# Optimization experiments

Measured on AMD Instinct MI355X. Metric: run time of the kernel, lower is better.

The kernel has to match this reference:

```python
import jax, jax.numpy as jnp
import numpy as np

NC, EC, NS, ES = 100000, 1600000, 50000, 800000
F_IN, H, G, OUT = 7, 64, 1024, 2
EPS = 1e-5


def setup_inputs() -> dict:
    key = jax.random.key(0)
    ks = jax.random.split(key, 24)
    d = {
        'x_c': jax.random.normal(ks[0], (NC, F_IN), jnp.float32),
        'edge_index_c': jax.random.randint(ks[1], (2, EC), 0, NC),
        'batch_c': jnp.sort(jax.random.randint(ks[2], (NC,), 0, G)),
        'x_s': jax.random.normal(ks[3], (NS, F_IN), jnp.float32),
        'edge_index_s': jax.random.randint(ks[4], (2, ES), 0, NS),
        'batch_s': jnp.sort(jax.random.randint(ks[5], (NS,), 0, G)),
    }
    def lin(k, i, o):
        return jax.random.normal(k, (i, o), jnp.float32) * (1.0 / np.sqrt(i))
    # chromo branch layers
    d['Wc0'] = lin(ks[6], F_IN, H); d['bc0'] = jnp.zeros((H,), jnp.float32)
    d['gc0'] = jnp.ones((H,), jnp.float32); d['betac0'] = jnp.zeros((H,), jnp.float32)
    d['Wc1'] = lin(ks[7], H, H); d['bc1'] = jnp.zeros((H,), jnp.float32)
    d['gc1'] = jnp.ones((H,), jnp.float32); d['betac1'] = jnp.zeros((H,), jnp.float32)
    # solvent branch layers
    d['Ws0'] = lin(ks[8], F_IN, H); d['bs0'] = jnp.zeros((H,), jnp.float32)
    d['gs0'] = jnp.ones((H,), jnp.float32); d['betas0'] = jnp.zeros((H,), jnp.float32)
    d['Ws1'] = lin(ks[9], H, H); d['bs1'] = jnp.zeros((H,), jnp.float32)
    d['gs1'] = jnp.ones((H,), jnp.float32); d['betas1'] = jnp.zeros((H,), jnp.float32)
    # heads
    d['Wf1'] = lin(ks[10], 2 * H, H); d['bf1'] = jnp.zeros((H,), jnp.float32)
    d['Wf2'] = lin(ks[11], H, OUT); d['bf2'] = jnp.zeros((OUT,), jnp.float32)
    return d


def _gcn(x, src, dst, W, b):
    # PyG GCNConv: add self-loops, symmetric D^-1/2 (A+I) D^-1/2 normalization
    N = x.shape[0]
    xw = x @ W
    si = jnp.concatenate([src, jnp.arange(N)])
    di = jnp.concatenate([dst, jnp.arange(N)])
    deg = jax.ops.segment_sum(jnp.ones(si.shape[0], x.dtype), di, num_segments=N)
    dinv = jnp.where(deg > 0, jax.lax.rsqrt(jnp.maximum(deg, 1.0)), 0.0)
    msg = xw[si] * (dinv[si] * dinv[di])[:, None]
    return jax.ops.segment_sum(msg, di, num_segments=N) + b


def _bn_relu(x, g, b):
    mu = x.mean(0)
    var = x.var(0)
    return jax.nn.relu((x - mu) * jax.lax.rsqrt(var + EPS) * g + b)


def _branch(x, ei, batch, layers):
    for (W, b, g, bt) in layers:
        x = _bn_relu(_gcn(x, ei[0], ei[1], W, b), g, bt)
    s = jax.ops.segment_sum(x, batch, num_segments=G)
    cnt = jax.ops.segment_sum(jnp.ones(x.shape[0], x.dtype), batch, num_segments=G)
    return s / jnp.maximum(cnt, 1.0)[:, None]  # global_mean_pool


def reference(x_c, edge_index_c, batch_c, x_s, edge_index_s, batch_s,
              Wc0, bc0, gc0, betac0, Wc1, bc1, gc1, betac1,
              Ws0, bs0, gs0, betas0, Ws1, bs1, gs1, betas1,
              Wf1, bf1, Wf2, bf2):
    hc = _branch(x_c, edge_index_c, batch_c,
                 [(Wc0, bc0, gc0, betac0), (Wc1, bc1, gc1, betac1)])
    hs = _branch(x_s, edge_index_s, batch_s,
                 [(Ws0, bs0, gs0, betas0), (Ws1, bs1, gs1, betas1)])
    h = jnp.concatenate([hc, hs], axis=1)  # [G, 2H]
    h = jax.nn.relu(h @ Wf1 + bf1)
    return h @ Wf2 + bf2  # [G, 2]
```

## Files before the change

### kernel.cpp

```cpp
#include <hip/hip_runtime.h>
#include <hip/hip_bf16.h>

typedef __hip_bfloat16 bf16;
typedef __attribute__((ext_vector_type(8))) short short8;
typedef __attribute__((ext_vector_type(4))) float f32x4;

#define NC_ 100000
#define EC_ 1600000
#define NS_ 50000
#define ES_ 800000
#define G_  1024
#define EPS_ 1e-5f

#define NB_C 782
#define NB_S 391
#define NBMAX 782
#define KSL 16
#define CSR_WC 2000400
#define CSR_WS 1000208

#define WS_MIN_FALLBACK 39356176ull
#define WS_BIG          52163344ull

__device__ __forceinline__ float b2f(bf16 v) { return __bfloat162float(v); }

__device__ __forceinline__ unsigned short f2bfbits(float v) {
    bf16 b = __float2bfloat16(v);
    union { bf16 b; unsigned short u; } c; c.b = b; return c.u;
}

__device__ __forceinline__ void acc8(float* a, uint4 r) {
    a[0] += __uint_as_float(r.x << 16); a[1] += __uint_as_float(r.x & 0xffff0000u);
    a[2] += __uint_as_float(r.y << 16); a[3] += __uint_as_float(r.y & 0xffff0000u);
    a[4] += __uint_as_float(r.z << 16); a[5] += __uint_as_float(r.z & 0xffff0000u);
    a[6] += __uint_as_float(r.w << 16); a[7] += __uint_as_float(r.w & 0xffff0000u);
}

__global__ void DualGNN_31327491457689_kernel() {}

__global__ __launch_bounds__(256) void k_fillout(float* out, float val, int n) {
    int i = blockIdx.x * 256 + threadIdx.x;
    if (i < n) out[i] = val;
}

__global__ __launch_bounds__(256) void k_zero(int* p, int n) {
    int i = blockIdx.x * 256 + threadIdx.x;
    int stride = gridDim.x * 256;
    while (i < n) { p[i] = 0; i += stride; }
}

__global__ __launch_bounds__(256) void k_bhist2(const int* dst_c, int* bcnt_c,
                                                const int* dst_s, int* bcnt_s) {
    __shared__ int h[NBMAX];
    int t = threadIdx.x;
    const int* dst; int* bcnt; int E, NB, b0, nb;
    if (blockIdx.x < 256) { dst = dst_c; bcnt = bcnt_c; E = EC_; NB = NB_C; b0 = blockIdx.x; nb = 256; }
    else { dst = dst_s; bcnt = bcnt_s; E = ES_; NB = NB_S; b0 = blockIdx.x - 256; nb = 128; }
    for (int i = t; i < NB; i += 256) h[i] = 0;
    __syncthreads();
    for (int e = b0 * 256 + t; e < E; e += nb * 256)
        atomicAdd(&h[dst[e] >> 7], 1);
    __syncthreads();
    for (int i = t; i < NB; i += 256) {
        int v = h[i];
        if (v) atomicAdd(&bcnt[i], v);
    }
}

__device__ void scan_one(const int* cnt, int* base, int* cur, int NB, int (*sc)[1024]) {
    int t = threadIdx.x;
    for (int i = t; i < 1024; i += 256) sc[0][i] = (i < NB) ? cnt[i] : 0;
    __syncthreads();
    int pin = 0;
    for (int off = 1; off < 1024; off <<= 1) {
        for (int i = t; i < 1024; i += 256) {
            int v = sc[pin][i];
            if (i >= off) v += sc[pin][i - off];
            sc[1 - pin][i] = v;
        }
        __syncthreads();
        pin ^= 1;
    }
    for (int i = t; i <= NB; i += 256) {
        int e = (i == 0) ? 0 : sc[pin][i - 1];
        base[i] = e;
        if (i < NB) cur[i] = e;
    }
    __syncthreads();
}

__global__ __launch_bounds__(256) void k_bscan(const int* cnt_c, int* base_c, int* cur_c, int NBc,
                                               const int* cnt_s, int* base_s, int* cur_s, int NBs) {
    __shared__ int sc[2][1024];
    scan_one(cnt_c, base_c, cur_c, NBc, sc);
    scan_one(cnt_s, base_s, cur_s, NBs, sc);
}

__global__ __launch_bounds__(256) void k_bin2(const int* ei_c, int* bcur_c, int* ebuf_c,
                                              const int* ei_s, int* bcur_s, int* ebuf_s) {
    __shared__ int cnt[NBMAX];
    __shared__ int slot[NBMAX * KSL];
    int t = threadIdx.x;
    const int *src, *dst; int *bcur, *ebuf; int E, NB; int base;
    if (blockIdx.x < 391) {
        src = ei_c; dst = ei_c + EC_; bcur = bcur_c; ebuf = ebuf_c;
        E = EC_; NB = NB_C; base = blockIdx.x * 4096;
    } else {
        src = ei_s; dst = ei_s + ES_; bcur = bcur_s; ebuf = ebuf_s;
        E = ES_; NB = NB_S; base = (blockIdx.x - 391) * 4096;
    }
    if (base >= E) return;
    for (int i = t; i < NB; i += 256) cnt[i] = 0;
    __syncthreads();
    int e1 = base + 4096;
    if (e1 > E) e1 = E;
    for (int e = base + t; e < e1; e += 256) {
        int d = dst[e];
        int p = ((d & 127) << 24) | src[e];
        int b = d >> 7;
        int sl = atomicAdd(&cnt[b], 1);
        if (sl < KSL) slot[b * KSL + sl] = p;
        else { int gp = atomicAdd(&bcur[b], 1); ebuf[gp] = p; }
    }
    __syncthreads();
    for (int b = t; b < NB; b += 256) {
        int c = cnt[b];
        if (c > KSL) c = KSL;
        if (c > 0) {
            int gp = atomicAdd(&bcur[b], c);
            for (int k = 0; k < c; k++) ebuf[gp + k] = slot[b * KSL + k];
        }
    }
}

__global__ __launch_bounds__(256) void k_build2(const int* bbase_c, const int* ebuf_c,
                                                const float* x_c, bf16* u_c,
                                                int* deg_c, int* start_c, int* csr_c,
                                                const int* bbase_s, const int* ebuf_s,
                                                const float* x_s, bf16* u_s,
                                                int* deg_s, int* start_s, int* csr_s) {
    __shared__ int lcnt[128], lofs[128], lcur[128];
    int t = threadIdx.x;
    const int* bbase; const int* ebuf; const float* x; bf16* u;
    int* deg; int* start; int* csr; int N, b;
    if (blockIdx.x < NB_C) {
        b = blockIdx.x; bbase = bbase_c; ebuf = ebuf_c; x = x_c; u = u_c;
        deg = deg_c; start = start_c; csr = csr_c; N = NC_;
    } else {
        b = blockIdx.x - NB_C; bbase = bbase_s; ebuf = ebuf_s; x = x_s; u = u_s;
        deg = deg_s; start = start_s; csr = csr_s; N = NS_;
    }
    int e0 = bbase[b], e1 = bbase[b + 1];
    int cb = ((e0 + 512 * b) + 3) & ~3;
    int n0 = b << 7;
    if (t < 128) lcnt[t] = 0;
    __syncthreads();
    for (int e = e0 + t; e < e1; e += 256)
        atomicAdd(&lcnt[((unsigned)ebuf[e]) >> 24], 1);
    __syncthreads();
    if (t < 64) {
        int c0 = lcnt[2 * t], c1 = lcnt[2 * t + 1];
        int v0 = (c0 + 3) & ~3, v1 = (c1 + 3) & ~3;
        int s = v0 + v1, incl = s;
        for (int off = 1; off < 64; off <<= 1) {
            int uu = __shfl_up(incl, off);
            if (t >= off) incl += uu;
        }
        int excl = incl - s;
        lofs[2 * t] = excl;
        lofs[2 * t + 1] = excl + v0;
    }
    __syncthreads();
    if (t < 128) {
        int node = n0 + t;
        if (node < N) {
            deg[node] = lcnt[t];
            start[node] = cb + lofs[t];
            if (x) {
                float d = rsqrtf((float)(lcnt[t] + 1));
                union __align__(16) Pack { bf16 hh[8]; uint4 v; } p;
                for (int k = 0; k < 7; k++) p.hh[k] = __float2bfloat16(x[node * 7 + k] * d);
                p.hh[7] = __float2bfloat16(0.f);
                ((uint4*)u)[node] = p.v;
            }
        }
        lcur[t] = lofs[t];
    }
    __syncthreads();
    if (t < 128) {
        int c = lcnt[t], al = (c + 3) & ~3;
        for (int k = c; k < al; k++) csr[cb + lofs[t] + k] = N;
    }
    for (int e = e0 + t; e < e1; e += 256) {
        unsigned p = (unsigned)ebuf[e];
        int dl = p >> 24;
        int pos = atomicAdd(&lcur[dl], 1);
        csr[cb + pos] = (int)(p & 0xFFFFFF);
    }
    if (b == 0 && t < 4 && u && x) ((int*)u)[N * 4 + t] = 0;
}

__global__ __launch_bounds__(256) void k_prep7(const float* x, const int* deg,
                                               bf16* u, int N) {
    int i = blockIdx.x * 256 + threadIdx.x;
    if (i > N) return;
    union __align__(16) Pack { bf16 hh[8]; uint4 v; } p;
    if (i == N) {
        p.v = (uint4){0u, 0u, 0u, 0u};
    } else {
        float d = rsqrtf((float)(deg[i] + 1));
        for (int k = 0; k < 7; k++) p.hh[k] = __float2bfloat16(x[i * 7 + k] * d);
        p.hh[7] = __float2bfloat16(0.f);
    }
    ((uint4*)u)[i] = p.v;
}

__global__ __launch_bounds__(256) void k_gather7m(
    const bf16* u_c, const int* csr_c, const int* start_c, const int* deg_c,
    const float* W_c, const float* bias_c, bf16* h_c, float* stat_c, int N_c,
    const bf16* u_s, const int* csr_s, const int* start_s, const int* deg_s,
    const float* W_s, const float* bias_s, bf16* h_s, float* stat_s, int N_s,
    int nblk_c) {
    __shared__ float Wsm[7 * 64];
    __shared__ float agg[128][9];
    __shared__ float sm[2][4][64];
    const bf16* u; const int *csr, *start, *deg; const float *W, *bias;
    bf16* h; float* stat; int N, lb;
    if ((int)blockIdx.x < nblk_c) {
        lb = blockIdx.x; u = u_c; csr = csr_c; start = start_c; deg = deg_c;
        W = W_c; bias = bias_c; h = h_c; stat = stat_c; N = N_c;
    } else {
        lb = blockIdx.x - nblk_c; u = u_s; csr = csr_s; start = start_s; deg = deg_s;
        W = W_s; bias = bias_s; h = h_s; stat = stat_s; N = N_s;
    }
    int t = threadIdx.x, lane = t & 63, ty = t >> 6;
    int team = t >> 1, par = t & 1;
    for (int i = t; i < 448; i += 256) Wsm[i] = W[i];
    float b = bias[lane];
    float sum = 0.f, sq = 0.f;
    const uint4* up = (const uint4*)u;
    int i = lb * 128 + team;
    float a[8] = {0.f, 0.f, 0.f, 0.f, 0.f, 0.f, 0.f, 0.f};
    if (i < N) {
        int dg = deg[i], s0 = start[i];
        int adeg = (dg + 3) & ~3;
        if (par == 0) acc8(a, up[i]);
        for (int j = 4 * par; j < adeg; j += 8) {
            uint4 nb = *(const uint4*)(csr + s0 + j);
            uint4 r0 = up[nb.x], r1 = up[nb.y], r2 = up[nb.z], r3 = up[nb.w];
            acc8(a, r0); acc8(a, r1); acc8(a, r2); acc8(a, r3);
        }
    }
    #pragma unroll
    for (int k = 0; k < 7; k++) a[k] += __shfl_xor(a[k], 1);
    if (i < N && par == 0) {
        float di = rsqrtf((float)(deg[i] + 1));
        #pragma unroll
        for (int k = 0; k < 7; k++) agg[team][k] = a[k] * di;
    }
    __syncthreads();
    int mbase = lb * 128 + ty * 32;
    for (int mm = 0; mm < 32; mm++) {
        int node = mbase + mm;
        if (node >= N) break;
        const float* ag = agg[ty * 32 + mm];
        float s = b;
        #pragma unroll
        for (int k = 0; k < 7; k++) s += ag[k] * Wsm[k * 64 + lane];
        h[(size_t)node * 64 + lane] = __float2bfloat16(s);
        sum += s; sq += s * s;
    }
    sm[0][ty][lane] = sum;
    sm[1][ty][lane] = sq;
    __syncthreads();
    if (ty == 0) {
        atomicAdd(&stat[lane],      sm[0][0][lane] + sm[0][1][lane] + sm[0][2][lane] + sm[0][3][lane]);
        atomicAdd(&stat[64 + lane], sm[1][0][lane] + sm[1][1][lane] + sm[1][2][lane] + sm[1][3][lane]);
    }
}

__global__ __launch_bounds__(256) void k_gemm1m(
    const bf16* h_c, const float* W_c, const float* stat_c, const float* gam_c,
    const float* bet_c, const int* deg_c, bf16* y_c, float invN_c, int N_c, int NY_c,
    const bf16* h_s, const float* W_s, const float* stat_s, const float* gam_s,
    const float* bet_s, const int* deg_s, bf16* y_s, float invN_s, int N_s, int NY_s,
    int nblk_c) {
    __shared__ short Wt[64][72];
    __shared__ float AB[128];
    const bf16* h; const float *W, *stat, *gam, *bet; const int* deg;
    bf16* y; float invN; int N, NY, lb, nb;
    if ((int)blockIdx.x < nblk_c) {
        lb = blockIdx.x; nb = nblk_c;
        h = h_c; W = W_c; stat = stat_c; gam = gam_c; bet = bet_c; deg = deg_c;
        y = y_c; invN = invN_c; N = N_c; NY = NY_c;
    } else {
        lb = blockIdx.x - nblk_c; nb = gridDim.x - nblk_c;
        h = h_s; W = W_s; stat = stat_s; gam = gam_s; bet = bet_s; deg = deg_s;
        y = y_s; invN = invN_s; N = N_s; NY = NY_s;
    }
    int t = threadIdx.x, lane = t & 63, ty = t >> 6;
    for (int i = t; i < 4096; i += 256) {
        int k = i >> 6, n = i & 63;
        Wt[n][k] = (short)f2bfbits(W[i]);
    }
    if (t < 64) {
        float mean = stat[t] * invN;
        float var = stat[64 + t] * invN - mean * mean;
        float A = gam[t] * rsqrtf(fmaxf(var, 0.f) + EPS_);
        AB[t] = A;
        AB[64 + t] = bet[t] - mean * A;
    }
    if (lb == 0 && t < 64) {
        int pr = t >> 4, cl = t & 15;
        y[((size_t)pr * NY + N) * 16 + cl] = __float2bfloat16(0.f);
    }
    __syncthreads();
    int quad = lane >> 4, l16 = lane & 15;
    short8 Bf[2][4];
    #pragma unroll
    for (int kt = 0; kt < 2; kt++)
        #pragma unroll
        for (int nt = 0; nt < 4; nt++) {
            int n = nt * 16 + l16, k0 = kt * 32 + quad * 8;
            Bf[kt][nt] = *(const short8*)&Wt[n][k0];
        }
    int ntile = (N + 63) >> 6;
    for (int tile = lb * 4 + ty; tile < ntile; tile += nb * 4) {
        int base = tile << 6;
        f32x4 acc[4][4];
        #pragma unroll
        for (int a = 0; a < 4; a++)
            #pragma unroll
            for (int b = 0; b < 4; b++) acc[a][b] = (f32x4){0.f, 0.f, 0.f, 0.f};
        #pragma unroll
        for (int kt = 0; kt < 2; kt++) {
            int k0 = kt * 32 + quad * 8;
            float Ak[8], Bk[8];
            #pragma unroll
            for (int j = 0; j < 8; j++) { Ak[j] = AB[k0 + j]; Bk[j] = AB[64 + k0 + j]; }
            #pragma unroll
            for (int mt = 0; mt < 4; mt++) {
                int node = base + mt * 16 + l16;
                uint4 raw = *(const uint4*)(h + (size_t)node * 64 + k0);
                unsigned rr[4] = {raw.x, raw.y, raw.z, raw.w};
                short8 af;
                #pragma unroll
                for (int j = 0; j < 8; j++) {
                    unsigned bits = (j & 1) ? (rr[j >> 1] & 0xffff0000u)
                                            : (rr[j >> 1] << 16);
                    float v = __uint_as_float(bits);
                    v = fmaxf(v * Ak[j] + Bk[j], 0.f);
                    af[j] = (short)f2bfbits(v);
                }
                #pragma unroll
                for (int nt = 0; nt < 4; nt++)
                    acc[mt][nt] = __builtin_amdgcn_mfma_f32_16x16x32_bf16(
                        af, Bf[kt][nt], acc[mt][nt], 0, 0, 0);
            }
        }
        #pragma unroll
        for (int mt = 0; mt < 4; mt++)
            #pragma unroll
            for (int r = 0; r < 4; r++) {
                int node = base + mt * 16 + quad * 4 + r;
                if (node < N) {
                    float dinv = rsqrtf((float)(deg[node] + 1));
                    #pragma unroll
                    for (int nt = 0; nt < 4; nt++)
                        y[((size_t)nt * NY + node) * 16 + l16] =
                            __float2bfloat16(acc[mt][nt][r] * dinv);
                }
            }
    }
}

__global__ __launch_bounds__(256) void k_gather16(const bf16* y, const int* csr,
                                                  const int* start, const int* deg,
                                                  const float* bias, bf16* h,
                                                  float* stat, int N, int NY) {
    __shared__ float sms[4][2][2][8];
    int t = threadIdx.x, lane = t & 63, ty = t >> 6;
    int team = lane >> 1, par = lane & 1;
    int pair = blockIdx.x & 3;
    int grp = blockIdx.x >> 2;
    int ngrp = gridDim.x >> 2;
    const uint4* yp = (const uint4*)y + (size_t)pair * NY * 2;
    uint4* hp = (uint4*)h + (size_t)pair * NY * 2;
    float b[8];
    #pragma unroll
    for (int k = 0; k < 8; k++) b[k] = bias[pair * 16 + par * 8 + k];
    float sum[8], sq[8];
    #pragma unroll
    for (int k = 0; k < 8; k++) { sum[k] = 0.f; sq[k] = 0.f; }
    for (int i = grp * 128 + ty * 32 + team; i < N; i += ngrp * 128) {
        int dg = deg[i], s0 = start[i];
        int adeg = (dg + 3) & ~3;
        float a[8];
        #pragma unroll
        for (int k = 0; k < 8; k++) a[k] = 0.f;
        acc8(a, yp[2 * i + par]);
        for (int j = 0; j < adeg; j += 4) {
            uint4 nb = *(const uint4*)(csr + s0 + j);
            uint4 q0 = yp[2 * nb.x + par];
            uint4 q1 = yp[2 * nb.y + par];
            uint4 q2 = yp[2 * nb.z + par];
            uint4 q3 = yp[2 * nb.w + par];
            acc8(a, q0); acc8(a, q1); acc8(a, q2); acc8(a, q3);
        }
        float di = rsqrtf((float)(dg + 1));
        union __align__(16) Pack { bf16 hh[8]; uint4 v; } p;
        #pragma unroll
        for (int k = 0; k < 8; k++) {
            float v = a[k] * di + b[k];
            p.hh[k] = __float2bfloat16(v);
            sum[k] += v; sq[k] += v * v;
        }
        hp[2 * i + par] = p.v;
    }
    #pragma unroll
    for (int k = 0; k < 8; k++) {
        float s1 = sum[k], s2 = sq[k];
        s1 += __shfl_down(s1, 32); s2 += __shfl_down(s2, 32);
        s1 += __shfl_down(s1, 16); s2 += __shfl_down(s2, 16);
        s1 += __shfl_down(s1, 8);  s2 += __shfl_down(s2, 8);
        s1 += __shfl_down(s1, 4);  s2 += __shfl_down(s2, 4);
        s1 += __shfl_down(s1, 2);  s2 += __shfl_down(s2, 2);
        if (lane < 2) { sms[ty][lane][0][k] = s1; sms[ty][lane][1][k] = s2; }
    }
    __syncthreads();
    if (t < 16) {
        int pp = t >> 3, k = t & 7;
        atomicAdd(&stat[pair * 16 + pp * 8 + k],
                  sms[0][pp][0][k] + sms[1][pp][0][k] + sms[2][pp][0][k] + sms[3][pp][0][k]);
    } else if (t >= 64 && t < 80) {
        int q = t - 64, pp = q >> 3, k = q & 7;
        atomicAdd(&stat[64 + pair * 16 + pp * 8 + k],
                  sms[0][pp][1][k] + sms[1][pp][1][k] + sms[2][pp][1][k] + sms[3][pp][1][k]);
    }
}

__global__ __launch_bounds__(256) void k_poolm(
    const bf16* h_c, const float* stat_c, const float* gam_c, const float* bet_c,
    const int* batch_c, float* pooled_c, float* cnt_c, float invN_c, int N_c, int NY_c,
    const bf16* h_s, const float* stat_s, const float* gam_s, const float* bet_s,
    const int* batch_s, float* pooled_s, float* cnt_s, float invN_s, int N_s, int NY_s,
    int nblk_c) {
    const bf16* h; const float *stat, *gam, *bet; const int* batch;
    float *pooled, *cnt; float invN; int N, NY, lb, nb;
    if ((int)blockIdx.x < nblk_c) {
        lb = blockIdx.x; nb = nblk_c;
        h = h_c; stat = stat_c; gam = gam_c; bet = bet_c; batch = batch_c;
        pooled = pooled_c; cnt = cnt_c; invN = invN_c; N = N_c; NY = NY_c;
    } else {
        lb = blockIdx.x - nblk_c; nb = gridDim.x - nblk_c;
        h = h_s; stat = stat_s; gam = gam_s; bet = bet_s; batch = batch_s;
        pooled = pooled_s; cnt = cnt_s; invN = invN_s; N = N_s; NY = NY_s;
    }
    int t = threadIdx.x;
    int lane = t & 63;
    float mean = stat[lane] * invN;
    float var = stat[64 + lane] * invN - mean * mean;
    float A = gam[lane] * rsqrtf(fmaxf(var, 0.f) + EPS_);
    float B = bet[lane] - mean * A;
    size_t pbase = (size_t)(lane >> 4) * NY * 16 + (lane & 15);
    int w = (lb * 256 + t) >> 6;
    int nw = nb * 4;
    int chunk = (N + nw - 1) / nw;
    int i0 = w * chunk;
    int i1 = i0 + chunk;
    if (i1 > N) i1 = N;
    if (i0 >= N) return;
    int curg = batch[i0];
    float acc = 0.f, c = 0.f;
    for (int i = i0; i < i1; i++) {
        int g = batch[i];
        if (g != curg) {
            atomicAdd(&pooled[(size_t)curg * 64 + lane], acc);
            if (lane == 0) atomicAdd(&cnt[curg], c);
            curg = g; acc = 0.f; c = 0.f;
        }
        acc += fmaxf(b2f(h[pbase + (size_t)i * 16]) * A + B, 0.f);
        c += 1.f;
    }
    atomicAdd(&pooled[(size_t)curg * 64 + lane], acc);
    if (lane == 0) atomicAdd(&cnt[curg], c);
}

__global__ __launch_bounds__(64) void k_head(const float* pooled_c, const float* cnt_c,
                                             const float* pooled_s, const float* cnt_s,
                                             const float* Wf1, const float* bf1_,
                                             const float* Wf2, const float* bf2_,
                                             float* out) {
    __shared__ float W1sm[128 * 64];
    __shared__ float W2sm[128];
    int t = threadIdx.x;
    for (int i = t; i < 128 * 64; i += 64) W1sm[i] = Wf1[i];
    for (int i = t; i < 128; i += 64) W2sm[i] = Wf2[i];
    __syncthreads();
    float bb1 = bf1_[t];
    float b20 = bf2_[0];
    float b21 = bf2_[1];
    for (int g = blockIdx.x; g < G_; g += gridDim.x) {
        float ic = 1.f / fmaxf(cnt_c[g], 1.f);
        float is = 1.f / fmaxf(cnt_s[g], 1.f);
        float hc = pooled_c[(size_t)g * 64 + t] * ic;
        float hs = pooled_s[(size_t)g * 64 + t] * is;
        float s = bb1;
        for (int k = 0; k < 64; k++) s += __shfl(hc, k) * W1sm[k * 64 + t];
        for (int k = 0; k < 64; k++) s += __shfl(hs, k) * W1sm[(64 + k) * 64 + t];
        s = fmaxf(s, 0.f);
        float p0 = s * W2sm[t * 2 + 0];
        float p1 = s * W2sm[t * 2 + 1];
        for (int off = 32; off > 0; off >>= 1) {
            p0 += __shfl_down(p0, off);
            p1 += __shfl_down(p1, off);
        }
        if (t == 0) {
            out[g * 2 + 0] = p0 + b20;
            out[g * 2 + 1] = p1 + b21;
        }
    }
}

extern "C" void kernel_launch(void* const* d_in, const int* in_sizes, int n_in,
                              void* d_out, int out_size, void* d_ws, size_t ws_size,
                              hipStream_t stream) {
    float* out = (float*)d_out;

    if (n_in != 26 || in_sizes[0] != NC_ * 7 || in_sizes[1] != 2 * EC_ ||
        in_sizes[2] != NC_ || in_sizes[3] != NS_ * 7 || in_sizes[4] != 2 * ES_ ||
        in_sizes[5] != NS_ || out_size != G_ * 2) {
        k_fillout<<<(out_size + 255) / 256, 256, 0, stream>>>(out, 7777.0f, out_size);
        return;
    }
    if (ws_size < (size_t)WS_MIN_FALLBACK) {
        k_fillout<<<(out_size + 255) / 256, 256, 0, stream>>>(
            out, 1000.0f + (float)(ws_size >> 20), out_size);
        return;
    }
    const bool big = (ws_size >= (size_t)WS_BIG);

    const float* x_c     = (const float*)d_in[0];
    const int*   ei_c    = (const int*)d_in[1];
    const int*   batch_c = (const int*)d_in[2];
    const float* x_s     = (const float*)d_in[3];
    const int*   ei_s    = (const int*)d_in[4];
    const int*   batch_s = (const int*)d_in[5];
    const float* Wc0  = (const float*)d_in[6];
    const float* bc0  = (const float*)d_in[7];
    const float* gc0  = (const float*)d_in[8];
    const float* bec0 = (const float*)d_in[9];
    const float* Wc1  = (const float*)d_in[10];
    const float* bc1  = (const float*)d_in[11];
    const float* gc1  = (const float*)d_in[12];
    const float* bec1 = (const float*)d_in[13];
    const float* Ws0  = (const float*)d_in[14];
    const float* bs0  = (const float*)d_in[15];
    const float* gs0  = (const float*)d_in[16];
    const float* bes0 = (const float*)d_in[17];
    const float* Ws1  = (const float*)d_in[18];
    const float* bs1  = (const float*)d_in[19];
    const float* gs1  = (const float*)d_in[20];
    const float* bes1 = (const float*)d_in[21];
    const float* Wf1  = (const float*)d_in[22];
    const float* bf1_ = (const float*)d_in[23];
    const float* Wf2  = (const float*)d_in[24];
    const float* bf2_ = (const float*)d_in[25];

    const int NYC = NC_ + 8;
    const int NYS = NS_ + 8;

    int* wsw = (int*)d_ws;
    size_t off = 0;
    float* stats_c  = (float*)(wsw + off); off += 256;
    float* stats_s  = (float*)(wsw + off); off += 256;
    float* pooled_c = (float*)(wsw + off); off += (size_t)G_ * 64;
    float* pooled_s = (float*)(wsw + off); off += (size_t)G_ * 64;
    float* cnt_c    = (float*)(wsw + off); off += G_;
    float* cnt_s    = (float*)(wsw + off); off += G_;
    int*   bcnt_c   = wsw + off; off += NB_C;
    int*   bcnt_s   = wsw + off; off += NB_S;
    size_t zero_words = off;
    int*   bbase_c  = wsw + off; off += NB_C + 1;
    int*   bcur_c   = wsw + off; off += NB_C;
    int*   bbase_s  = wsw + off; off += NB_S + 1;
    int*   bcur_s   = wsw + off; off += NB_S;
    int*   deg_c    = wsw + off; off += NC_;
    int*   start_c  = wsw + off; off += NC_;
    int*   deg_s    = wsw + off; off += NS_;
    int*   start_s  = wsw + off; off += NS_;
    int*   csr_c    = wsw + off; off += CSR_WC;
    int*   csr_s    = wsw + off; off += CSR_WS;
    off = (off + 3) & ~(size_t)3;

    k_zero<<<512, 256, 0, stream>>>(wsw, (int)zero_words);
    k_bhist2<<<384, 256, 0, stream>>>(ei_c + EC_, bcnt_c, ei_s + ES_, bcnt_s);
    k_bscan<<<1, 256, 0, stream>>>(bcnt_c, bbase_c, bcur_c, NB_C,
                                   bcnt_s, bbase_s, bcur_s, NB_S);

    if (big) {
        bf16* h_c = (bf16*)(wsw + off); off += 3201024;
        bf16* y_c = (bf16*)(wsw + off); off += 3200256;
        bf16* h_s = (bf16*)(wsw + off); off += 1601536;
        bf16* y_s = (bf16*)(wsw + off); off += 1600256;
        int*  ebuf_c = (int*)h_c;
        int*  ebuf_s = (int*)h_c + 1600000;
        bf16* u_c = y_c;
        bf16* u_s = y_s;

        k_bin2<<<587, 256, 0, stream>>>(ei_c, bcur_c, ebuf_c, ei_s, bcur_s, ebuf_s);
        k_build2<<<NB_C + NB_S, 256, 0, stream>>>(bbase_c, ebuf_c, x_c, u_c,
                                                  deg_c, start_c, csr_c,
                                                  bbase_s, ebuf_s, x_s, u_s,
                                                  deg_s, start_s, csr_s);
        k_gather7m<<<NB_C + NB_S, 256, 0, stream>>>(
            u_c, csr_c, start_c, deg_c, Wc0, bc0, h_c, stats_c, NC_,
            u_s, csr_s, start_s, deg_s, Ws0, bs0, h_s, stats_s, NS_, NB_C);
        k_gemm1m<<<768, 256, 0, stream>>>(
            h_c, Wc1, stats_c, gc0, bec0, deg_c, y_c, 1.0f / NC_, NC_, NYC,
            h_s, Ws1, stats_s, gs0, bes0, deg_s, y_s, 1.0f / NS_, NS_, NYS, 512);
        k_gather16<<<3128, 256, 0, stream>>>(y_c, csr_c, start_c, deg_c, bc1,
                                             h_c, stats_c + 128, NC_, NYC);
        k_gather16<<<1564, 256, 0, stream>>>(y_s, csr_s, start_s, deg_s, bs1,
                                             h_s, stats_s + 128, NS_, NYS);
        k_poolm<<<384, 256, 0, stream>>>(
            h_c, stats_c + 128, gc1, bec1, batch_c, pooled_c, cnt_c, 1.0f / NC_, NC_, NYC,
            h_s, stats_s + 128, gs1, bes1, batch_s, pooled_s, cnt_s, 1.0f / NS_, NS_, NYS, 256);
    } else {
        bf16* hbuf = (bf16*)(wsw + off); off += 3201024;
        bf16* ybuf = (bf16*)(wsw + off); off += 3200256;
        int*  ebuf_c = (int*)hbuf;
        int*  ebuf_s = (int*)hbuf + 1600000;
        bf16* ub = ybuf;

        k_bin2<<<587, 256, 0, stream>>>(ei_c, bcur_c, ebuf_c, ei_s, bcur_s, ebuf_s);
        k_build2<<<NB_C + NB_S, 256, 0, stream>>>(bbase_c, ebuf_c, x_c, ub,
                                                  deg_c, start_c, csr_c,
                                                  bbase_s, ebuf_s, (const float*)0, (bf16*)0,
                                                  deg_s, start_s, csr_s);
        k_gather7m<<<NB_C, 256, 0, stream>>>(
            ub, csr_c, start_c, deg_c, Wc0, bc0, hbuf, stats_c, NC_,
            ub, csr_c, start_c, deg_c, Wc0, bc0, hbuf, stats_c, NC_, NB_C);
        k_gemm1m<<<512, 256, 0, stream>>>(
            hbuf, Wc1, stats_c, gc0, bec0, deg_c, ybuf, 1.0f / NC_, NC_, NYC,
            hbuf, Wc1, stats_c, gc0, bec0, deg_c, ybuf, 1.0f / NC_, NC_, NYC, 512);
        k_gather16<<<3128, 256, 0, stream>>>(ybuf, csr_c, start_c, deg_c, bc1,
                                             hbuf, stats_c + 128, NC_, NYC);
        k_poolm<<<256, 256, 0, stream>>>(
            hbuf, stats_c + 128, gc1, bec1, batch_c, pooled_c, cnt_c, 1.0f / NC_, NC_, NYC,
            hbuf, stats_c + 128, gc1, bec1, batch_c, pooled_c, cnt_c, 1.0f / NC_, NC_, NYC, 256);
        k_prep7<<<(NS_ + 256) / 256, 256, 0, stream>>>(x_s, deg_s, ub, NS_);
        k_gather7m<<<NB_S, 256, 0, stream>>>(
            ub, csr_s, start_s, deg_s, Ws0, bs0, hbuf, stats_s, NS_,
            ub, csr_s, start_s, deg_s, Ws0, bs0, hbuf, stats_s, NS_, NB_S);
        k_gemm1m<<<256, 256, 0, stream>>>(
            hbuf, Ws1, stats_s, gs0, bes0, deg_s, ybuf, 1.0f / NS_, NS_, NYS,
            hbuf, Ws1, stats_s, gs0, bes0, deg_s, ybuf, 1.0f / NS_, NS_, NYS, 256);
        k_gather16<<<1564, 256, 0, stream>>>(ybuf, csr_s, start_s, deg_s, bs1,
                                             hbuf, stats_s + 128, NS_, NYS);
        k_poolm<<<256, 256, 0, stream>>>(
            hbuf, stats_s + 128, gs1, bes1, batch_s, pooled_s, cnt_s, 1.0f / NS_, NS_, NYS,
            hbuf, stats_s + 128, gs1, bes1, batch_s, pooled_s, cnt_s, 1.0f / NS_, NS_, NYS, 256);
    }

    k_head<<<128, 64, 0, stream>>>(pooled_c, cnt_c, pooled_s, cnt_s, Wf1, bf1_, Wf2, bf2_, out);
}
```

Before: 391.7 us.

## Switch y/h to node-major 64-wide rows and merge branch gather launches

Changes the intermediate feature layout from four 16-column planes to contiguous 64-column rows per node. Each gather then reads a full 128-byte row across 8 lanes with one pass over the CSR, instead of four passes split by blockIdx. The chromo and solvent layer-2 gathers are also fused into a single launch, and the workspace is rearranged so the zeroed region starts after the big buffers. The trade-off is fewer nodes per block per iteration and larger per-edge row fetches.

New measurement: 431.5 us. 10.1% more time.

```diff
diff --git a/kernel.cpp b/kernel.cpp
--- a/kernel.cpp
+++ b/kernel.cpp
@@ -298,6 +298,7 @@
         h = h_s; W = W_s; stat = stat_s; gam = gam_s; bet = bet_s; deg = deg_s;
         y = y_s; invN = invN_s; N = N_s; NY = NY_s;
     }
+    (void)NY;
     int t = threadIdx.x, lane = t & 63, ty = t >> 6;
     for (int i = t; i < 4096; i += 256) {
         int k = i >> 6, n = i & 63;
@@ -311,8 +312,7 @@
         AB[64 + t] = bet[t] - mean * A;
     }
     if (lb == 0 && t < 64) {
-        int pr = t >> 4, cl = t & 15;
-        y[((size_t)pr * NY + N) * 16 + cl] = __float2bfloat16(0.f);
+        y[(size_t)N * 64 + t] = __float2bfloat16(0.f);
     }
     __syncthreads();
     int quad = lane >> 4, l16 = lane & 15;
@@ -367,75 +367,80 @@
                     float dinv = rsqrtf((float)(deg[node] + 1));
                     #pragma unroll
                     for (int nt = 0; nt < 4; nt++)
-                        y[((size_t)nt * NY + node) * 16 + l16] =
+                        y[(size_t)node * 64 + nt * 16 + l16] =
                             __float2bfloat16(acc[mt][nt][r] * dinv);
                 }
             }
     }
 }
 
-__global__ __launch_bounds__(256) void k_gather16(const bf16* y, const int* csr,
-                                                  const int* start, const int* deg,
-                                                  const float* bias, bf16* h,
-                                                  float* stat, int N, int NY) {
-    __shared__ float sms[4][2][2][8];
+__global__ __launch_bounds__(256) void k_gather16m(
+    const bf16* y_c, const int* csr_c, const int* start_c, const int* deg_c,
+    const float* bias_c, bf16* h_c, float* stat_c, int N_c,
+    const bf16* y_s, const int* csr_s, const int* start_s, const int* deg_s,
+    const float* bias_s, bf16* h_s, float* stat_s, int N_s, int nblk_c) {
+    __shared__ float sms[2][4][64];
+    const bf16* y; const int *csr, *start, *deg; const float* bias;
+    bf16* h; float* stat; int N, lb, nb;
+    if ((int)blockIdx.x < nblk_c) {
+        lb = blockIdx.x; nb = nblk_c;
+        y = y_c; csr = csr_c; start = start_c; deg = deg_c; bias = bias_c;
+        h = h_c; stat = stat_c; N = N_c;
+    } else {
+        lb = blockIdx.x - nblk_c; nb = gridDim.x - nblk_c;
+        y = y_s; csr = csr_s; start = start_s; deg = deg_s; bias = bias_s;
+        h = h_s; stat = stat_s; N = N_s;
+    }
     int t = threadIdx.x, lane = t & 63, ty = t >> 6;
-    int team = lane >> 1, par = lane & 1;
-    int pair = blockIdx.x & 3;
-    int grp = blockIdx.x >> 2;
-    int ngrp = gridDim.x >> 2;
-    const uint4* yp = (const uint4*)y + (size_t)pair * NY * 2;
-    uint4* hp = (uint4*)h + (size_t)pair * NY * 2;
+    int k = lane & 7;
+    int tg = t >> 3;
+    const uint4* yp = (const uint4*)y;
+    uint4* hp = (uint4*)h;
     float b[8];
     #pragma unroll
-    for (int k = 0; k < 8; k++) b[k] = bias[pair * 16 + par * 8 + k];
+    for (int j = 0; j < 8; j++) b[j] = bias[k * 8 + j];
     float sum[8], sq[8];
     #pragma unroll
-    for (int k = 0; k < 8; k++) { sum[k] = 0.f; sq[k] = 0.f; }
-    for (int i = grp * 128 + ty * 32 + team; i < N; i += ngrp * 128) {
+    for (int j = 0; j < 8; j++) { sum[j] = 0.f; sq[j] = 0.f; }
+    for (int i = lb * 32 + tg; i < N; i += nb * 32) {
         int dg = deg[i], s0 = start[i];
         int adeg = (dg + 3) & ~3;
         float a[8];
         #pragma unroll
-        for (int k = 0; k < 8; k++) a[k] = 0.f;
-        acc8(a, yp[2 * i + par]);
+        for (int j = 0; j < 8; j++) a[j] = 0.f;
+        acc8(a, yp[(size_t)i * 8 + k]);
         for (int j = 0; j < adeg; j += 4) {
-            uint4 nb = *(const uint4*)(csr + s0 + j);
-            uint4 q0 = yp[2 * nb.x + par];
-            uint4 q1 = yp[2 * nb.y + par];
-            uint4 q2 = yp[2 * nb.z + par];
-            uint4 q3 = yp[2 * nb.w + par];
+            uint4 nb4 = *(const uint4*)(csr + s0 + j);
+            uint4 q0 = yp[(size_t)nb4.x * 8 + k];
+            uint4 q1 = yp[(size_t)nb4.y * 8 + k];
+            uint4 q2 = yp[(size_t)nb4.z * 8 + k];
+            uint4 q3 = yp[(size_t)nb4.w * 8 + k];
             acc8(a, q0); acc8(a, q1); acc8(a, q2); acc8(a, q3);
         }
         float di = rsqrtf((float)(dg + 1));
         union __align__(16) Pack { bf16 hh[8]; uint4 v; } p;
         #pragma unroll
-        for (int k = 0; k < 8; k++) {
-            float v = a[k] * di + b[k];
-            p.hh[k] = __float2bfloat16(v);
-            sum[k] += v; sq[k] += v * v;
-        }
-        hp[2 * i + par] = p.v;
+        for (int j = 0; j < 8; j++) {
+            float v = a[j] * di + b[j];
+            p.hh[j] = __float2bfloat16(v);
+            sum[j] += v; sq[j] += v * v;
+        }
+        hp[(size_t)i * 8 + k] = p.v;
     }
     #pragma unroll
-    for (int k = 0; k < 8; k++) {
-        float s1 = sum[k], s2 = sq[k];
+    for (int j = 0; j < 8; j++) {
+        float s1 = sum[j], s2 = sq[j];
         s1 += __shfl_down(s1, 32); s2 += __shfl_down(s2, 32);
         s1 += __shfl_down(s1, 16); s2 += __shfl_down(s2, 16);
         s1 += __shfl_down(s1, 8);  s2 += __shfl_down(s2, 8);
-        s1 += __shfl_down(s1, 4);  s2 += __shfl_down(s2, 4);
-        s1 += __shfl_down(s1, 2);  s2 += __shfl_down(s2, 2);
-        if (lane < 2) { sms[ty][lane][0][k] = s1; sms[ty][lane][1][k] = s2; }
-    }
-    __syncthreads();
-    if (t < 16) {
-        int pp = t >> 3, k = t & 7;
-        atomicAdd(&stat[pair * 16 + pp * 8 + k],
-                  sms[0][pp][0][k] + sms[1][pp][0][k] + sms[2][pp][0][k] + sms[3][pp][0][k]);
-    } else if (t >= 64 && t < 80) {
-        int q = t - 64, pp = q >> 3, k = q & 7;
-        atomicAdd(&stat[64 + pair * 16 + pp * 8 + k],
-                  sms[0][pp][1][k] + sms[1][pp][1][k] + sms[2][pp][1][k] + sms[3][pp][1][k]);
+        if (lane < 8) { sms[0][ty][lane * 8 + j] = s1; sms[1][ty][lane * 8 + j] = s2; }
+    }
+    __syncthreads();
+    if (t < 64) {
+        atomicAdd(&stat[t], sms[0][0][t] + sms[0][1][t] + sms[0][2][t] + sms[0][3][t]);
+    } else if (t >= 128 && t < 192) {
+        int c = t - 128;
+        atomicAdd(&stat[64 + c], sms[1][0][c] + sms[1][1][c] + sms[1][2][c] + sms[1][3][c]);
     }
 }
 
@@ -456,13 +461,13 @@
         h = h_s; stat = stat_s; gam = gam_s; bet = bet_s; batch = batch_s;
         pooled = pooled_s; cnt = cnt_s; invN = invN_s; N = N_s; NY = NY_s;
     }
+    (void)NY;
     int t = threadIdx.x;
     int lane = t & 63;
     float mean = stat[lane] * invN;
     float var = stat[64 + lane] * invN - mean * mean;
     float A = gam[lane] * rsqrtf(fmaxf(var, 0.f) + EPS_);
     float B = bet[lane] - mean * A;
-    size_t pbase = (size_t)(lane >> 4) * NY * 16 + (lane & 15);
     int w = (lb * 256 + t) >> 6;
     int nw = nb * 4;
     int chunk = (N + nw - 1) / nw;
@@ -479,7 +484,7 @@
             if (lane == 0) atomicAdd(&cnt[curg], c);
             curg = g; acc = 0.f; c = 0.f;
         }
-        acc += fmaxf(b2f(h[pbase + (size_t)i * 16]) * A + B, 0.f);
+        acc += fmaxf(b2f(h[(size_t)i * 64 + lane]) * A + B, 0.f);
         c += 1.f;
     }
     atomicAdd(&pooled[(size_t)curg * 64 + lane], acc);
@@ -571,7 +576,8 @@
     const int NYS = NS_ + 8;
 
     int* wsw = (int*)d_ws;
-    size_t off = 0;
+    size_t off = big ? (size_t)(3201024 + 3200256 + 1601536 + 1600256)
+                     : (size_t)(3201024 + 3200256);
     float* stats_c  = (float*)(wsw + off); off += 256;
     float* stats_s  = (float*)(wsw + off); off += 256;
     float* pooled_c = (float*)(wsw + off); off += (size_t)G_ * 64;
@@ -580,7 +586,7 @@
     float* cnt_s    = (float*)(wsw + off); off += G_;
     int*   bcnt_c   = wsw + off; off += NB_C;
     int*   bcnt_s   = wsw + off; off += NB_S;
-    size_t zero_words = off;
+    const int zero_words = 256 + 256 + G_ * 64 * 2 + G_ * 2 + NB_C + NB_S;
     int*   bbase_c  = wsw + off; off += NB_C + 1;
     int*   bcur_c   = wsw + off; off += NB_C;
     int*   bbase_s  = wsw + off; off += NB_S + 1;
@@ -591,18 +597,17 @@
     int*   start_s  = wsw + off; off += NS_;
     int*   csr_c    = wsw + off; off += CSR_WC;
     int*   csr_s    = wsw + off; off += CSR_WS;
-    off = (off + 3) & ~(size_t)3;
-
-    k_zero<<<512, 256, 0, stream>>>(wsw, (int)zero_words);
+
+    k_zero<<<512, 256, 0, stream>>>((int*)stats_c, zero_words);
     k_bhist2<<<384, 256, 0, stream>>>(ei_c + EC_, bcnt_c, ei_s + ES_, bcnt_s);
     k_bscan<<<1, 256, 0, stream>>>(bcnt_c, bbase_c, bcur_c, NB_C,
                                    bcnt_s, bbase_s, bcur_s, NB_S);
 
     if (big) {
-        bf16* h_c = (bf16*)(wsw + off); off += 3201024;
-        bf16* y_c = (bf16*)(wsw + off); off += 3200256;
-        bf16* h_s = (bf16*)(wsw + off); off += 1601536;
-        bf16* y_s = (bf16*)(wsw + off); off += 1600256;
+        bf16* h_c = (bf16*)wsw;
+        bf16* y_c = (bf16*)(wsw + 3201024);
+        bf16* h_s = (bf16*)(wsw + 3201024 + 3200256);
+        bf16* y_s = (bf16*)(wsw + 3201024 + 3200256 + 1601536);
         int*  ebuf_c = (int*)h_c;
         int*  ebuf_s = (int*)h_c + 1600000;
         bf16* u_c = y_c;
@@ -619,16 +624,15 @@
         k_gemm1m<<<768, 256, 0, stream>>>(
             h_c, Wc1, stats_c, gc0, bec0, deg_c, y_c, 1.0f / NC_, NC_, NYC,
             h_s, Ws1, stats_s, gs0, bes0, deg_s, y_s, 1.0f / NS_, NS_, NYS, 512);
-        k_gather16<<<3128, 256, 0, stream>>>(y_c, csr_c, start_c, deg_c, bc1,
-                                             h_c, stats_c + 128, NC_, NYC);
-        k_gather16<<<1564, 256, 0, stream>>>(y_s, csr_s, start_s, deg_s, bs1,
-                                             h_s, stats_s + 128, NS_, NYS);
+        k_gather16m<<<3128 + 1564, 256, 0, stream>>>(
+            y_c, csr_c, start_c, deg_c, bc1, h_c, stats_c + 128, NC_,
+            y_s, csr_s, start_s, deg_s, bs1, h_s, stats_s + 128, NS_, 3128);
         k_poolm<<<384, 256, 0, stream>>>(
             h_c, stats_c + 128, gc1, bec1, batch_c, pooled_c, cnt_c, 1.0f / NC_, NC_, NYC,
             h_s, stats_s + 128, gs1, bes1, batch_s, pooled_s, cnt_s, 1.0f / NS_, NS_, NYS, 256);
     } else {
-        bf16* hbuf = (bf16*)(wsw + off); off += 3201024;
-        bf16* ybuf = (bf16*)(wsw + off); off += 3200256;
+        bf16* hbuf = (bf16*)wsw;
+        bf16* ybuf = (bf16*)(wsw + 3201024);
         int*  ebuf_c = (int*)hbuf;
         int*  ebuf_s = (int*)hbuf + 1600000;
         bf16* ub = ybuf;
@@ -644,8 +648,9 @@
         k_gemm1m<<<512, 256, 0, stream>>>(
             hbuf, Wc1, stats_c, gc0, bec0, deg_c, ybuf, 1.0f / NC_, NC_, NYC,
             hbuf, Wc1, stats_c, gc0, bec0, deg_c, ybuf, 1.0f / NC_, NC_, NYC, 512);
-        k_gather16<<<3128, 256, 0, stream>>>(ybuf, csr_c, start_c, deg_c, bc1,
-                                             hbuf, stats_c + 128, NC_, NYC);
+        k_gather16m<<<3128, 256, 0, stream>>>(
+            ybuf, csr_c, start_c, deg_c, bc1, hbuf, stats_c + 128, NC_,
+            ybuf, csr_c, start_c, deg_c, bc1, hbuf, stats_c + 128, NC_, 3128);
         k_poolm<<<256, 256, 0, stream>>>(
             hbuf, stats_c + 128, gc1, bec1, batch_c, pooled_c, cnt_c, 1.0f / NC_, NC_, NYC,
             hbuf, stats_c + 128, gc1, bec1, batch_c, pooled_c, cnt_c, 1.0f / NC_, NC_, NYC, 256);
@@ -656,8 +661,9 @@
         k_gemm1m<<<256, 256, 0, stream>>>(
             hbuf, Ws1, stats_s, gs0, bes0, deg_s, ybuf, 1.0f / NS_, NS_, NYS,
             hbuf, Ws1, stats_s, gs0, bes0, deg_s, ybuf, 1.0f / NS_, NS_, NYS, 256);
-        k_gather16<<<1564, 256, 0, stream>>>(ybuf, csr_s, start_s, deg_s, bs1,
-                                             hbuf, stats_s + 128, NS_, NYS);
+        k_gather16m<<<1564, 256, 0, stream>>>(
+            ybuf, csr_s, start_s, deg_s, bs1, hbuf, stats_s + 128, NS_,
+            ybuf, csr_s, start_s, deg_s, bs1, hbuf, stats_s + 128, NS_, 1564);
         k_poolm<<<256, 256, 0, stream>>>(
             hbuf, stats_s + 128, gs1, bes1, batch_s, pooled_s, cnt_s, 1.0f / NS_, NS_, NYS,
             hbuf, stats_s + 128, gs1, bes1, batch_s, pooled_s, cnt_s, 1.0f / NS_, NS_, NYS, 256);
```
